# Kernel optimization log

Measured on AMD Instinct MI355X. Metric: run time of the kernel, lower is better.

The kernel has to match this reference:

```python
import jax, jax.numpy as jnp
import numpy as np

N = 100000      # nodes
E = 300000      # edges
D_IN = 32       # input feature dim
D_MEM = 256     # memory dim
D_HID = 256     # hidden dim
D_TIME = 32     # time encoding dim
HEADS = 4
C = D_HID // 4  # per-head channels (GATConv out_channels)
D_OUT = 2


def gru_cell(x, h, wih, whh, bih, bhh):
    # torch.nn.GRUCell semantics, gate order (r, z, n)
    gi = x @ wih.T + bih
    gh = h @ whh.T + bhh
    ir, iz, inn = jnp.split(gi, 3, axis=-1)
    hr, hz, hn = jnp.split(gh, 3, axis=-1)
    r = jax.nn.sigmoid(ir + hr)
    z = jax.nn.sigmoid(iz + hz)
    n = jnp.tanh(inn + r * hn)
    return (1.0 - z) * n + z * h


def gat_layer(h, src, dst, W, a_src, a_dst, bias):
    # PyG GATConv(concat=True), default add_self_loops=True, negative_slope=0.2
    n = h.shape[0]
    xh = (h @ W.T).reshape(n, HEADS, C)              # [N,H,C]
    al_s = (xh * a_src).sum(-1)                      # [N,H]
    al_d = (xh * a_dst).sum(-1)                      # [N,H]
    loop = jnp.arange(n, dtype=src.dtype)
    s = jnp.concatenate([src, loop])
    d = jnp.concatenate([dst, loop])
    e = jax.nn.leaky_relu(al_s[s] + al_d[d], 0.2)    # [E+N,H]
    emax = jax.ops.segment_max(e, d, num_segments=n)
    ee = jnp.exp(e - emax[d])
    denom = jax.ops.segment_sum(ee, d, num_segments=n)
    alpha = ee / denom[d]                            # softmax over incoming edges
    out = jax.ops.segment_sum(alpha[:, :, None] * xh[s], d, num_segments=n)
    return out.reshape(n, HEADS * C) + bias


def setup_inputs() -> dict:
    key = jax.random.key(0)
    ks = jax.random.split(key, 32)
    w = lambda k, sh: jax.random.normal(k, sh, jnp.float32) * 0.05
    d_msg_in = 2 * D_MEM + D_IN + D_TIME  # 576
    return {
        "x": jax.random.normal(ks[0], (N, D_IN), jnp.float32),
        "timestamps": jax.random.uniform(ks[1], (E,), jnp.float32),
        "node_memory": jnp.zeros((N, D_MEM), jnp.float32),
        "last_update_time": jnp.zeros((N,), jnp.float32),
        "msg_w1": w(ks[2], (D_HID, d_msg_in)), "msg_b1": w(ks[3], (D_HID,)),
        "msg_w2": w(ks[4], (D_MEM, D_HID)), "msg_b2": w(ks[5], (D_MEM,)),
        "time_w1": w(ks[6], (D_TIME, 1)), "time_b1": w(ks[7], (D_TIME,)),
        "time_w2": w(ks[8], (D_TIME, D_TIME)), "time_b2": w(ks[9], (D_TIME,)),
        "gru_wih": w(ks[10], (3 * D_MEM, D_MEM)), "gru_whh": w(ks[11], (3 * D_MEM, D_MEM)),
        "gru_bih": w(ks[12], (3 * D_MEM,)), "gru_bhh": w(ks[13], (3 * D_MEM,)),
        "gat1_w": w(ks[14], (HEADS * C, D_MEM)), "gat1_asrc": w(ks[15], (HEADS, C)),
        "gat1_adst": w(ks[16], (HEADS, C)), "gat1_b": w(ks[17], (HEADS * C,)),
        "gat2_w": w(ks[18], (HEADS * C, D_HID)), "gat2_asrc": w(ks[19], (HEADS, C)),
        "gat2_adst": w(ks[20], (HEADS, C)), "gat2_b": w(ks[21], (HEADS * C,)),
        "cls_w1": w(ks[22], (D_HID // 2, D_HID)), "cls_b1": w(ks[23], (D_HID // 2,)),
        "cls_w2": w(ks[24], (D_OUT, D_HID // 2)), "cls_b2": w(ks[25], (D_OUT,)),
        "edge_index": jax.random.randint(ks[26], (2, E), 0, N, jnp.int32),
        "batch": jnp.zeros((N,), jnp.int32),
    }


def reference(x, timestamps, node_memory, last_update_time,
              msg_w1, msg_b1, msg_w2, msg_b2,
              time_w1, time_b1, time_w2, time_b2,
              gru_wih, gru_whh, gru_bih, gru_bhh,
              gat1_w, gat1_asrc, gat1_adst, gat1_b,
              gat2_w, gat2_asrc, gat2_adst, gat2_b,
              cls_w1, cls_b1, cls_w2, cls_b2,
              edge_index, batch):
    src, dst = edge_index[0], edge_index[1]
    edge_attr = x[src]                               # torch path: edge_attr=None -> x[edge_index[0]]
    current_time = timestamps.max()
    # --- compute_messages ---
    dt = (current_time - jnp.maximum(last_update_time[src], last_update_time[dst]))[:, None]
    te = jax.nn.relu(dt @ time_w1.T + time_b1) @ time_w2.T + time_b2
    mi = jnp.concatenate([node_memory[src], node_memory[dst], edge_attr, te], axis=-1)  # [E,576]
    msgs = jax.nn.relu(mi @ msg_w1.T + msg_b1) @ msg_w2.T + msg_b2                      # [E,256]
    # --- update_memory: fused segment-mean + batched GRU ---
    counts = jax.ops.segment_sum(jnp.ones((E,), msgs.dtype), dst, num_segments=N)
    agg = jax.ops.segment_sum(msgs, dst, num_segments=N) / jnp.maximum(counts, 1.0)[:, None]
    mem_new = gru_cell(agg, node_memory, gru_wih, gru_whh, gru_bih, gru_bhh)
    mem = jnp.where((counts > 0)[:, None], mem_new, node_memory)
    # --- GAT embedding layers (dropout inactive in eval) ---
    h = jax.nn.elu(gat_layer(mem, src, dst, gat1_w, gat1_asrc, gat1_adst, gat1_b))
    h = jax.nn.elu(gat_layer(h, src, dst, gat2_w, gat2_asrc, gat2_adst, gat2_b))
    # --- global mean pool (single graph, batch==0) + classifier ---
    gsum = jax.ops.segment_sum(h, batch, num_segments=1)
    gcnt = jax.ops.segment_sum(jnp.ones((N,), h.dtype), batch, num_segments=1)
    g = gsum / gcnt[:, None]
    logits = jax.nn.relu(g @ cls_w1.T + cls_b1) @ cls_w2.T + cls_b2
    return logits
```

## Files before the change

### kernel.cpp

```cpp
#include <hip/hip_runtime.h>

#define NN 100000
#define NE 300000
#define GPLANE 528

typedef float f32x4 __attribute__((ext_vector_type(4)));
typedef __bf16 bf16x8 __attribute__((ext_vector_type(8)));
typedef unsigned short ushort8v __attribute__((ext_vector_type(8)));

__device__ __forceinline__ int enc_f(float f) {
    int i = __float_as_int(f);
    return i >= 0 ? i : (i ^ 0x7fffffff);
}
__device__ __forceinline__ float dec_f(int i) {
    return __int_as_float(i >= 0 ? i : (i ^ 0x7fffffff));
}
__device__ __forceinline__ unsigned short f2bf(float f) {
    unsigned u = __float_as_uint(f);
    u += 0x7fffu + ((u >> 16) & 1u);
    return (unsigned short)(u >> 16);
}
__device__ __forceinline__ float bf2f(unsigned short u) {
    return __uint_as_float((unsigned)u << 16);
}

__global__ void k_dbg(float* out, float v) { out[0] = v; out[1] = v; }

__global__ void k_fill_i32(int* p, int v, int n) {
    int i = blockIdx.x * 256 + threadIdx.x;
    if (i < n) p[i] = v;
}

__global__ void k_pack_w_sub(const float* __restrict__ src, unsigned short* __restrict__ dst,
                             int OUT, int K, int stride, int off) {
    int i = blockIdx.x * 256 + threadIdx.x;
    if (i >= OUT * K) return;
    int o = i / K, k = i % K;
    int ob = o >> 6, n = (o >> 4) & 3, fr = o & 15;
    int step = k >> 5, kq = (k >> 3) & 3, j = k & 7;
    size_t dsti = ((((size_t)step * (OUT >> 6) + ob) * 4 + n) * 64 + (kq * 16 + fr)) * 8 + j;
    dst[dsti] = f2bf(src[(size_t)o * stride + off + k]);
}

__global__ void k_fold_te(const float* __restrict__ msg_w1, const float* __restrict__ tw2,
                          const float* __restrict__ tb2, const float* __restrict__ b1,
                          float* __restrict__ Mtd, float* __restrict__ b1eff) {
    int i = blockIdx.x * 256 + threadIdx.x;
    if (i < 256 * 32) {
        int o = i >> 5, col = i & 31;
        float s = 0.f;
        const float* w1d = msg_w1 + (size_t)o * 576 + 544;
#pragma unroll
        for (int c = 0; c < 32; ++c) s += w1d[c] * tw2[c * 32 + col];
        Mtd[i] = s;
        if (col == 0) {
            float sb = b1[o];
#pragma unroll
            for (int c = 0; c < 32; ++c) sb += w1d[c] * tb2[c];
            b1eff[o] = sb;
        }
    }
}

__global__ void k_timemax(const float* __restrict__ ts, int n, int* out) {
    float m = -INFINITY;
    int stride = gridDim.x * blockDim.x;
    for (int i = blockIdx.x * blockDim.x + threadIdx.x; i < n; i += stride)
        m = fmaxf(m, ts[i]);
    atomicMax(out, enc_f(m));
}

__global__ void k_counts(const int* __restrict__ ei, float* __restrict__ counts) {
    int stride = gridDim.x * blockDim.x;
    for (int i = blockIdx.x * blockDim.x + threadIdx.x; i < NE; i += stride)
        atomicAdd(&counts[ei[NE + i]], 1.f);
}

__global__ void k_scan1(const float* __restrict__ counts, int* __restrict__ rowptr,
                        int* __restrict__ bsum) {
    __shared__ int sh[256];
    int t = threadIdx.x;
    int i = blockIdx.x * 256 + t;
    int v = (i < NN) ? ((int)counts[i] + 1) : 0;
    sh[t] = v;
    __syncthreads();
    for (int off = 1; off < 256; off <<= 1) {
        int x = (t >= off) ? sh[t - off] : 0;
        __syncthreads();
        sh[t] += x;
        __syncthreads();
    }
    if (i < NN) rowptr[i + 1] = sh[t];
    if (t == 255) bsum[blockIdx.x] = sh[255];
}

__global__ void k_scan2(int* __restrict__ bsum, int nb) {
    __shared__ int sh[512];
    int t = threadIdx.x;
    sh[t] = (t < nb) ? bsum[t] : 0;
    __syncthreads();
    for (int off = 1; off < 512; off <<= 1) {
        int x = (t >= off) ? sh[t - off] : 0;
        __syncthreads();
        sh[t] += x;
        __syncthreads();
    }
    if (t < nb) bsum[t] = sh[t];
}

__global__ void k_scan3(int* __restrict__ rowptr, const int* __restrict__ bsum,
                        int* __restrict__ fillp, int* __restrict__ fillE) {
    int i = blockIdx.x * 256 + threadIdx.x;
    if (i == 0) {
        rowptr[0] = 0;
        fillp[0] = 0;
        fillE[0] = 0;
    }
    if (i < NN) {
        int b = i >> 8;
        int off = b > 0 ? bsum[b - 1] : 0;
        int v = rowptr[i + 1] + off;
        rowptr[i + 1] = v;
        if (i + 1 < NN) {
            fillp[i + 1] = v;
            fillE[i + 1] = v - (i + 1);
        }
    }
}

__global__ void k_csr_fill(const int* __restrict__ ei, int* __restrict__ fill,
                           int* __restrict__ colidx) {
    int i = blockIdx.x * 256 + threadIdx.x;
    if (i < NE) {
        int d = ei[NE + i];
        int pos = atomicAdd(&fill[d], 1);
        colidx[pos] = ei[i];
    } else if (i < NE + NN) {
        int n = i - NE;
        int pos = atomicAdd(&fill[n], 1);
        colidx[pos] = n;
    }
}

__global__ void k_ecsr_fill(const int* __restrict__ ei, int* __restrict__ fillE,
                            int* __restrict__ esrc, int* __restrict__ edst) {
    int i = blockIdx.x * 256 + threadIdx.x;
    if (i < NE) {
        int d = ei[NE + i];
        int pos = atomicAdd(&fillE[d], 1);
        esrc[pos] = ei[i];
        edst[pos] = d;
    }
}

__global__ __launch_bounds__(512, 4) void k_pre1(
    const float* __restrict__ mem, const float* __restrict__ x,
    const unsigned short* __restrict__ w1ap, const unsigned short* __restrict__ w1bp,
    const unsigned short* __restrict__ w1cp,
    unsigned short* __restrict__ P13, unsigned short* __restrict__ P2,
    unsigned short* __restrict__ membf) {
    __shared__ unsigned short Af[2 * 8 * GPLANE];
    __shared__ unsigned short Axf[2 * 512];
    const int t = threadIdx.x;
    const int lane = t & 63, w = t >> 6;
    const int row0 = blockIdx.x * 32;
    const int frow = lane & 15, hi = lane >> 4;
    const int half = w >> 2, cq = w & 3;

    {
        int sr = t >> 4, sq = t & 15;
        int row = row0 + sr;
        const float* pm = mem + (size_t)row * 256 + sq * 16;
        int smq = sr >> 4, sfr = sr & 15;
#pragma unroll
        for (int j2 = 0; j2 < 2; ++j2) {
            int k8 = sq * 16 + j2 * 8;
            int st = k8 >> 5, kq = (k8 >> 3) & 3;
            float4 m0 = *(const float4*)(pm + j2 * 8);
            float4 m1 = *(const float4*)(pm + j2 * 8 + 4);
            ushort8v um;
            um[0] = f2bf(m0.x); um[1] = f2bf(m0.y); um[2] = f2bf(m0.z); um[3] = f2bf(m0.w);
            um[4] = f2bf(m1.x); um[5] = f2bf(m1.y); um[6] = f2bf(m1.z); um[7] = f2bf(m1.w);
            *(ushort8v*)&Af[((smq * 8) + st) * GPLANE + (kq * 16 + sfr) * 8] = um;
            *(ushort8v*)(membf + (size_t)row * 256 + k8) = um;
        }
    }
    if (t < 128) {
        int sr = t >> 2, sq = t & 3;
        int row = row0 + sr;
        const float* px = x + (size_t)row * 32 + sq * 8;
        float4 v0 = *(const float4*)px, v1 = *(const float4*)(px + 4);
        ushort8v u;
        u[0] = f2bf(v0.x); u[1] = f2bf(v0.y); u[2] = f2bf(v0.z); u[3] = f2bf(v0.w);
        u[4] = f2bf(v1.x); u[5] = f2bf(v1.y); u[6] = f2bf(v1.z); u[7] = f2bf(v1.w);
        *(ushort8v*)&Axf[(sr >> 4) * 512 + (sq * 16 + (sr & 15)) * 8] = u;
    }
    __syncthreads();

    f32x4 acc[2][4];
#pragma unroll
    for (int mf = 0; mf < 2; ++mf)
#pragma unroll
        for (int c = 0; c < 4; ++c) acc[mf][c] = (f32x4){0, 0, 0, 0};

    const unsigned short* wp = half ? w1bp : w1ap;
    for (int step = 0; step < 8; ++step) {
        bf16x8 aA[2];
#pragma unroll
        for (int mf = 0; mf < 2; ++mf)
            aA[mf] = *(const bf16x8*)&Af[((mf * 8) + step) * GPLANE + lane * 8];
#pragma unroll
        for (int ctl = 0; ctl < 4; ++ctl) {
            bf16x8 b = *(const bf16x8*)(wp + (((size_t)step * 4 + cq) * 4 + ctl) * 512 + lane * 8);
#pragma unroll
            for (int mf = 0; mf < 2; ++mf)
                acc[mf][ctl] = __builtin_amdgcn_mfma_f32_16x16x32_bf16(aA[mf], b, acc[mf][ctl], 0, 0, 0);
        }
    }
    if (half == 0) {
        bf16x8 aX[2];
#pragma unroll
        for (int mf = 0; mf < 2; ++mf)
            aX[mf] = *(const bf16x8*)&Axf[mf * 512 + lane * 8];
#pragma unroll
        for (int ctl = 0; ctl < 4; ++ctl) {
            bf16x8 b = *(const bf16x8*)(w1cp + (((size_t)0 * 4 + cq) * 4 + ctl) * 512 + lane * 8);
#pragma unroll
            for (int mf = 0; mf < 2; ++mf)
                acc[mf][ctl] = __builtin_amdgcn_mfma_f32_16x16x32_bf16(aX[mf], b, acc[mf][ctl], 0, 0, 0);
        }
    }
    unsigned short* P = half ? P2 : P13;
#pragma unroll
    for (int mf = 0; mf < 2; ++mf)
#pragma unroll
        for (int ctl = 0; ctl < 4; ++ctl) {
            int col = cq * 64 + ctl * 16 + frow;
#pragma unroll
            for (int r = 0; r < 4; ++r) {
                int row = row0 + mf * 16 + hi * 4 + r;
                P[(size_t)row * 256 + col] = f2bf(acc[mf][ctl][r]);
            }
        }
}

__global__ __launch_bounds__(512, 4) void k_msg_mfma(
    const int* __restrict__ ct, const float* __restrict__ lut,
    const int* __restrict__ esrc, const int* __restrict__ edst,
    const unsigned short* __restrict__ P13, const unsigned short* __restrict__ P2,
    const unsigned short* __restrict__ wtdp, const float* __restrict__ b1eff,
    const unsigned short* __restrict__ w2p, const float* __restrict__ b2,
    const float* __restrict__ tw1, const float* __restrict__ tb1,
    float* __restrict__ agg) {
    __shared__ unsigned short As[64][40];
    __shared__ unsigned short Hs[64][264];
    __shared__ int Da[64];

    const int t = threadIdx.x;
    const int lane = t & 63, wave = t >> 6;
    const int row0 = blockIdx.x * 64;
    const int frow = lane & 15;
    const int fk = (lane >> 4) * 8;
    const int hi = lane >> 4;
    const int wb = wave >> 1;
    const int wn = (wave & 1) * 2;

    if (t < 64) {
        int e = row0 + t;
        Da[t] = (e < NE) ? edst[e] : -1;
    }

    const int srow = t >> 3;
    const int sj = t & 7;
    const int eIdx = row0 + srow;
    const bool ev = eIdx < NE;
    const int s_e = ev ? esrc[eIdx] : 0;
    const int d_e = ev ? edst[eIdx] : 0;

    {
        float ctv = dec_f(*ct);
        float dt = ev ? (ctv - fmaxf(lut[s_e], lut[d_e])) : 0.f;
        ushort4 u;
        int c0 = sj * 4;
        u.x = f2bf(fmaxf(dt * tw1[c0 + 0] + tb1[c0 + 0], 0.f));
        u.y = f2bf(fmaxf(dt * tw1[c0 + 1] + tb1[c0 + 1], 0.f));
        u.z = f2bf(fmaxf(dt * tw1[c0 + 2] + tb1[c0 + 2], 0.f));
        u.w = f2bf(fmaxf(dt * tw1[c0 + 3] + tb1[c0 + 3], 0.f));
        *(ushort4*)&As[srow][c0] = u;
    }
#pragma unroll
    for (int q = 0; q < 4; ++q) {
        int c = sj * 8 + q * 64;
        ushort4 a0 = *(const ushort4*)(P13 + (size_t)s_e * 256 + c);
        ushort4 a1 = *(const ushort4*)(P13 + (size_t)s_e * 256 + c + 4);
        ushort4 b0 = *(const ushort4*)(P2 + (size_t)d_e * 256 + c);
        ushort4 b1v = *(const ushort4*)(P2 + (size_t)d_e * 256 + c + 4);
        ushort8v u;
        u[0] = f2bf(bf2f(a0.x) + bf2f(b0.x)); u[1] = f2bf(bf2f(a0.y) + bf2f(b0.y));
        u[2] = f2bf(bf2f(a0.z) + bf2f(b0.z)); u[3] = f2bf(bf2f(a0.w) + bf2f(b0.w));
        u[4] = f2bf(bf2f(a1.x) + bf2f(b1v.x)); u[5] = f2bf(bf2f(a1.y) + bf2f(b1v.y));
        u[6] = f2bf(bf2f(a1.z) + bf2f(b1v.z)); u[7] = f2bf(bf2f(a1.w) + bf2f(b1v.w));
        *(ushort8v*)&Hs[srow][c] = u;
    }
    __syncthreads();

    f32x4 acc[4][2];
#pragma unroll
    for (int m = 0; m < 4; m++)
#pragma unroll
        for (int n = 0; n < 2; n++) acc[m][n] = (f32x4){0.f, 0.f, 0.f, 0.f};

    {
        bf16x8 a[4];
#pragma unroll
        for (int m = 0; m < 4; m++)
            a[m] = *(const bf16x8*)&As[m * 16 + frow][fk];
#pragma unroll
        for (int n = 0; n < 2; n++) {
            bf16x8 b = *(const bf16x8*)(wtdp + (((size_t)0 * 4 + wb) * 4 + (wn + n)) * 512 + lane * 8);
#pragma unroll
            for (int m = 0; m < 4; m++)
                acc[m][n] = __builtin_amdgcn_mfma_f32_16x16x32_bf16(a[m], b, acc[m][n], 0, 0, 0);
        }
    }
#pragma unroll
    for (int n = 0; n < 2; n++) {
        int c = wave * 32 + n * 16 + frow;
        float bb = b1eff[c];
#pragma unroll
        for (int m = 0; m < 4; m++) {
#pragma unroll
            for (int r = 0; r < 4; r++) {
                int rr = m * 16 + hi * 4 + r;
                float v = acc[m][n][r] + bf2f(Hs[rr][c]) + bb;
                Hs[rr][c] = f2bf(fmaxf(v, 0.f));
            }
            acc[m][n] = (f32x4){0.f, 0.f, 0.f, 0.f};
        }
    }
    __syncthreads();

    bf16x8 bnext[2];
#pragma unroll
    for (int n = 0; n < 2; n++)
        bnext[n] = *(const bf16x8*)(w2p + (((size_t)0 * 4 + wb) * 4 + (wn + n)) * 512 + lane * 8);
    for (int step = 0; step < 8; ++step) {
        const int k0 = step * 32;
        bf16x8 bcur[2];
#pragma unroll
        for (int n = 0; n < 2; n++) bcur[n] = bnext[n];
        if (step < 7) {
#pragma unroll
            for (int n = 0; n < 2; n++)
                bnext[n] = *(const bf16x8*)(w2p + (((size_t)(step + 1) * 4 + wb) * 4 + (wn + n)) * 512 + lane * 8);
        }
        bf16x8 a[4];
#pragma unroll
        for (int m = 0; m < 4; m++)
            a[m] = *(const bf16x8*)&Hs[m * 16 + frow][k0 + fk];
#pragma unroll
        for (int m = 0; m < 4; m++)
#pragma unroll
            for (int n = 0; n < 2; n++)
                acc[m][n] = __builtin_amdgcn_mfma_f32_16x16x32_bf16(a[m], bcur[n], acc[m][n], 0, 0, 0);
    }

    __syncthreads();
    {
        float bb2[2];
#pragma unroll
        for (int n = 0; n < 2; n++) bb2[n] = b2[wave * 32 + n * 16 + frow];
#pragma unroll
        for (int m = 0; m < 4; m++) {
            int rbase = m * 16 + hi * 4;
#pragma unroll
            for (int r = 0; r < 4; r++) {
#pragma unroll
                for (int n = 0; n < 2; n++)
                    Hs[rbase + r][wave * 32 + n * 16 + frow] = f2bf(acc[m][n][r] + bb2[n]);
            }
        }
        __syncthreads();

        int nrows = min(64, NE - row0);
        int col = t & 255;
        int rs = (t >> 8) * 32;
        int re = min(nrows, rs + 32);
        if (rs < re) {
            float run = 0.f;
            int cur = Da[rs];
            for (int i = rs; i < re; ++i) {
                int d = Da[i];
                if (d != cur) {
                    atomicAdd(agg + (size_t)cur * 256 + col, run);
                    run = 0.f;
                    cur = d;
                }
                run += bf2f(Hs[i][col]);
            }
            atomicAdd(agg + (size_t)cur * 256 + col, run);
        }
    }
}

__global__ __launch_bounds__(512, 4) void k_gru_mfma(
    const float* __restrict__ agg, const unsigned short* __restrict__ membf,
    const float* __restrict__ counts,
    const unsigned short* __restrict__ pwih, const unsigned short* __restrict__ pwhh,
    const float* __restrict__ bih, const float* __restrict__ bhh,
    unsigned short* __restrict__ memout) {
    __shared__ unsigned short Af[2 * 2 * 8 * GPLANE];
    const int t = threadIdx.x;
    const int lane = t & 63, w = t >> 6;
    const int row0 = blockIdx.x * 32;
    const int frow = lane & 15, hi = lane >> 4;
    const int cqp = blockIdx.y * 2 + (w >> 2);
    const int ctl = w & 3;

    {
        int sr = t >> 4, sq = t & 15;
        int row = row0 + sr;
        float inv = 1.f / fmaxf(counts[row], 1.f);
        const float* pa = agg + (size_t)row * 256 + sq * 16;
        const unsigned short* pm = membf + (size_t)row * 256 + sq * 16;
        int smq = sr >> 4, sfr = sr & 15;
#pragma unroll
        for (int j2 = 0; j2 < 2; ++j2) {
            int k8 = sq * 16 + j2 * 8;
            int st = k8 >> 5, kq = (k8 >> 3) & 3;
            float4 a0 = *(const float4*)(pa + j2 * 8);
            float4 a1 = *(const float4*)(pa + j2 * 8 + 4);
            ushort8v um = *(const ushort8v*)(pm + j2 * 8);
            ushort8v ua;
            ua[0] = f2bf(a0.x * inv); ua[1] = f2bf(a0.y * inv); ua[2] = f2bf(a0.z * inv); ua[3] = f2bf(a0.w * inv);
            ua[4] = f2bf(a1.x * inv); ua[5] = f2bf(a1.y * inv); ua[6] = f2bf(a1.z * inv); ua[7] = f2bf(a1.w * inv);
            int pos = kq * 16 + sfr;
            *(ushort8v*)&Af[(((0 * 2 + smq) * 8) + st) * GPLANE + pos * 8] = ua;
            *(ushort8v*)&Af[(((1 * 2 + smq) * 8) + st) * GPLANE + pos * 8] = um;
        }
    }
    __syncthreads();

    f32x4 rpre[2], zpre[2], inn[2], hn[2];
#pragma unroll
    for (int mf = 0; mf < 2; ++mf) {
        rpre[mf] = (f32x4){0, 0, 0, 0};
        zpre[mf] = (f32x4){0, 0, 0, 0};
        inn[mf]  = (f32x4){0, 0, 0, 0};
        hn[mf]   = (f32x4){0, 0, 0, 0};
    }

    for (int step = 0; step < 8; ++step) {
        bf16x8 aA[2], aM[2];
#pragma unroll
        for (int mf = 0; mf < 2; ++mf) {
            aA[mf] = *(const bf16x8*)&Af[(((0 * 2 + mf) * 8) + step) * GPLANE + lane * 8];
            aM[mf] = *(const bf16x8*)&Af[(((1 * 2 + mf) * 8) + step) * GPLANE + lane * 8];
        }
        size_t o_r = (((size_t)step * 12 + 0 * 4 + cqp) * 4 + ctl) * 512 + lane * 8;
        size_t o_z = (((size_t)step * 12 + 1 * 4 + cqp) * 4 + ctl) * 512 + lane * 8;
        size_t o_n = (((size_t)step * 12 + 2 * 4 + cqp) * 4 + ctl) * 512 + lane * 8;
        bf16x8 bIr = *(const bf16x8*)(pwih + o_r);
        bf16x8 bHr = *(const bf16x8*)(pwhh + o_r);
        bf16x8 bIz = *(const bf16x8*)(pwih + o_z);
        bf16x8 bHz = *(const bf16x8*)(pwhh + o_z);
        bf16x8 bIn = *(const bf16x8*)(pwih + o_n);
        bf16x8 bHn = *(const bf16x8*)(pwhh + o_n);
#pragma unroll
        for (int mf = 0; mf < 2; ++mf) {
            rpre[mf] = __builtin_amdgcn_mfma_f32_16x16x32_bf16(aA[mf], bIr, rpre[mf], 0, 0, 0);
            rpre[mf] = __builtin_amdgcn_mfma_f32_16x16x32_bf16(aM[mf], bHr, rpre[mf], 0, 0, 0);
            zpre[mf] = __builtin_amdgcn_mfma_f32_16x16x32_bf16(aA[mf], bIz, zpre[mf], 0, 0, 0);
            zpre[mf] = __builtin_amdgcn_mfma_f32_16x16x32_bf16(aM[mf], bHz, zpre[mf], 0, 0, 0);
            inn[mf]  = __builtin_amdgcn_mfma_f32_16x16x32_bf16(aA[mf], bIn, inn[mf], 0, 0, 0);
            hn[mf]   = __builtin_amdgcn_mfma_f32_16x16x32_bf16(aM[mf], bHn, hn[mf], 0, 0, 0);
        }
    }

    const int col = cqp * 64 + ctl * 16 + frow;
    const float br = bih[col] + bhh[col];
    const float bz = bih[256 + col] + bhh[256 + col];
    const float bin = bih[512 + col];
    const float bhn = bhh[512 + col];
#pragma unroll
    for (int mf = 0; mf < 2; ++mf)
#pragma unroll
        for (int r = 0; r < 4; ++r) {
            int row = row0 + mf * 16 + hi * 4 + r;
            float cnt = counts[row];
            float rg = 1.f / (1.f + expf(-(rpre[mf][r] + br)));
            float zg = 1.f / (1.f + expf(-(zpre[mf][r] + bz)));
            float ng = tanhf(inn[mf][r] + bin + rg * (hn[mf][r] + bhn));
            int pos = ((col >> 3) & 3) * 16 + (hi * 4 + r);
            float hp = bf2f(Af[(((1 * 2 + mf) * 8) + (col >> 5)) * GPLANE + pos * 8 + (col & 7)]);
            memout[(size_t)row * 256 + col] = f2bf((cnt > 0.f) ? ((1.f - zg) * ng + zg * hp) : hp);
        }
}

__global__ __launch_bounds__(256, 4) void k_xh_mfma(
    const unsigned short* __restrict__ A, const unsigned short* __restrict__ wp,
    const float* __restrict__ asrc, const float* __restrict__ adst,
    unsigned short* __restrict__ xh, float* __restrict__ als, float* __restrict__ ald) {
    const int t = threadIdx.x;
    const int lane = t & 63, w = t >> 6;
    const int row0 = blockIdx.x * 64;
    const int frow = lane & 15, fk = (lane >> 4) * 8, hi = lane >> 4;

    f32x4 acc[4][4];
#pragma unroll
    for (int m = 0; m < 4; m++)
#pragma unroll
        for (int c = 0; c < 4; c++) acc[m][c] = (f32x4){0, 0, 0, 0};

    for (int step = 0; step < 8; ++step) {
        const int k0 = step * 32;
        bf16x8 a[4];
#pragma unroll
        for (int m = 0; m < 4; ++m) {
            int row = min(row0 + m * 16 + frow, NN - 1);
            a[m] = *(const bf16x8*)(A + (size_t)row * 256 + k0 + fk);
        }
#pragma unroll
        for (int ctl = 0; ctl < 4; ++ctl) {
            bf16x8 b = *(const bf16x8*)(wp + (((size_t)step * 4 + w) * 4 + ctl) * 512 + lane * 8);
#pragma unroll
            for (int m = 0; m < 4; ++m)
                acc[m][ctl] = __builtin_amdgcn_mfma_f32_16x16x32_bf16(a[m], b, acc[m][ctl], 0, 0, 0);
        }
    }

    float asv[4], adv[4];
#pragma unroll
    for (int ctl = 0; ctl < 4; ++ctl) {
        asv[ctl] = asrc[w * 64 + ctl * 16 + frow];
        adv[ctl] = adst[w * 64 + ctl * 16 + frow];
    }
#pragma unroll
    for (int m = 0; m < 4; ++m) {
        float ps[4] = {0, 0, 0, 0}, pd[4] = {0, 0, 0, 0};
#pragma unroll
        for (int ctl = 0; ctl < 4; ++ctl) {
            int col = w * 64 + ctl * 16 + frow;
#pragma unroll
            for (int r = 0; r < 4; ++r) {
                float v = acc[m][ctl][r];
                ps[r] += v * asv[ctl];
                pd[r] += v * adv[ctl];
                int row = row0 + m * 16 + hi * 4 + r;
                if (row < NN) xh[(size_t)row * 256 + col] = f2bf(v);
            }
        }
#pragma unroll
        for (int off = 1; off < 16; off <<= 1) {
#pragma unroll
            for (int r = 0; r < 4; ++r) {
                ps[r] += __shfl_xor(ps[r], off, 64);
                pd[r] += __shfl_xor(pd[r], off, 64);
            }
        }
        if (frow == 0) {
#pragma unroll
            for (int r = 0; r < 4; ++r) {
                int row = row0 + m * 16 + hi * 4 + r;
                if (row < NN) { als[row * 4 + w] = ps[r]; ald[row * 4 + w] = pd[r]; }
            }
        }
    }
}

__global__ __launch_bounds__(256) void k_gat_csr(
    const int* __restrict__ rowptr, const int* __restrict__ colidx,
    const float* __restrict__ als, const float* __restrict__ ald,
    const unsigned short* __restrict__ xh, const float* __restrict__ bias,
    unsigned short* __restrict__ outb) {
    int d = blockIdx.x * 4 + (threadIdx.x >> 6);
    if (d >= NN) return;
    int lane = threadIdx.x & 63;
    int h = lane >> 4;
    int beg = rowptr[d], end = rowptr[d + 1];
    float aldv = ald[d * 4 + h];

    float m = -INFINITY;
    for (int p = beg; p < end; ++p) {
        int s = colidx[p];
        float e = als[s * 4 + h] + aldv;
        e = e > 0.f ? e : 0.2f * e;
        m = fmaxf(m, e);
    }
    float den = 0.f;
    float a0 = 0.f, a1 = 0.f, a2 = 0.f, a3 = 0.f;
    for (int p = beg; p < end; ++p) {
        int s = colidx[p];
        float e = als[s * 4 + h] + aldv;
        e = e > 0.f ? e : 0.2f * e;
        float pw = expf(e - m);
        den += pw;
        ushort4 uv = *(const ushort4*)(xh + (size_t)s * 256 + lane * 4);
        a0 += pw * bf2f(uv.x);
        a1 += pw * bf2f(uv.y);
        a2 += pw * bf2f(uv.z);
        a3 += pw * bf2f(uv.w);
    }
    float inv = 1.f / den;
    int c = lane * 4;
    float4 bv = *(const float4*)(bias + c);
    float ox = a0 * inv + bv.x; ox = ox > 0.f ? ox : expm1f(ox);
    float oy = a1 * inv + bv.y; oy = oy > 0.f ? oy : expm1f(oy);
    float oz = a2 * inv + bv.z; oz = oz > 0.f ? oz : expm1f(oz);
    float ow = a3 * inv + bv.w; ow = ow > 0.f ? ow : expm1f(ow);
    ushort4 o;
    o.x = f2bf(ox); o.y = f2bf(oy); o.z = f2bf(oz); o.w = f2bf(ow);
    *(ushort4*)(outb + (size_t)d * 256 + c) = o;
}

__global__ __launch_bounds__(256) void k_pool(const unsigned short* __restrict__ h,
                                              const int* __restrict__ batch, float* __restrict__ gsum) {
    int t = threadIdx.x;
    const int per = (NN + gridDim.x - 1) / gridDim.x;
    int n0 = blockIdx.x * per, n1 = min(NN, n0 + per);
    float s = 0.f, cnt = 0.f;
    for (int n = n0; n < n1; n++) {
        if (batch[n] == 0) {
            s += bf2f(h[(size_t)n * 256 + t]);
            cnt += 1.f;
        }
    }
    atomicAdd(&gsum[t], s);
    if (t == 0) atomicAdd(&gsum[256], cnt);
}

__global__ void k_cls(const float* __restrict__ gsum, const float* __restrict__ w1,
                      const float* __restrict__ b1, const float* __restrict__ w2,
                      const float* __restrict__ b2, float* __restrict__ out) {
    __shared__ float g[256];
    __shared__ float hid[128];
    int t = threadIdx.x;
    float gc = gsum[256];
    g[t] = gsum[t] / gc;
    __syncthreads();
    if (t < 128) {
        float s = b1[t];
        for (int k = 0; k < 256; k++) s += g[k] * w1[t * 256 + k];
        hid[t] = fmaxf(s, 0.f);
    }
    __syncthreads();
    if (t < 2) {
        float s = b2[t];
        for (int k = 0; k < 128; k++) s += hid[k] * w2[t * 128 + k];
        out[t] = s;
    }
}

extern "C" void kernel_launch(void* const* d_in, const int* in_sizes, int n_in,
                              void* d_out, int out_size, void* d_ws, size_t ws_size,
                              hipStream_t stream) {
    const float* xv      = (const float*)d_in[0];
    const float* tsv     = (const float*)d_in[1];
    const float* nodemem = (const float*)d_in[2];
    const float* lut     = (const float*)d_in[3];
    const float* msg_w1  = (const float*)d_in[4];
    const float* msg_b1  = (const float*)d_in[5];
    const float* msg_w2  = (const float*)d_in[6];
    const float* msg_b2  = (const float*)d_in[7];
    const float* time_w1 = (const float*)d_in[8];
    const float* time_b1 = (const float*)d_in[9];
    const float* time_w2 = (const float*)d_in[10];
    const float* time_b2 = (const float*)d_in[11];
    const float* gru_wih = (const float*)d_in[12];
    const float* gru_whh = (const float*)d_in[13];
    const float* gru_bih = (const float*)d_in[14];
    const float* gru_bhh = (const float*)d_in[15];
    const float* gat1_w    = (const float*)d_in[16];
    const float* gat1_asrc = (const float*)d_in[17];
    const float* gat1_adst = (const float*)d_in[18];
    const float* gat1_b    = (const float*)d_in[19];
    const float* gat2_w    = (const float*)d_in[20];
    const float* gat2_asrc = (const float*)d_in[21];
    const float* gat2_adst = (const float*)d_in[22];
    const float* gat2_b    = (const float*)d_in[23];
    const float* cls_w1 = (const float*)d_in[24];
    const float* cls_b1 = (const float*)d_in[25];
    const float* cls_w2 = (const float*)d_in[26];
    const float* cls_b2 = (const float*)d_in[27];
    const int* ei    = (const int*)d_in[28];
    const int* batch = (const int*)d_in[29];
    float* out = (float*)d_out;

    char* wsb = (char*)d_ws;
    size_t off = 0;
    auto carve = [&](size_t bytes) {
        char* p = wsb + off;
        off += (bytes + 255) & ~(size_t)255;
        return p;
    };
    int*   curtime = (int*)carve(4);
    unsigned short* w1ap = (unsigned short*)carve((size_t)256 * 256 * 2);
    unsigned short* w1bp = (unsigned short*)carve((size_t)256 * 256 * 2);
    unsigned short* w1cp = (unsigned short*)carve((size_t)256 * 32 * 2);
    unsigned short* wtdp = (unsigned short*)carve((size_t)256 * 32 * 2);
    unsigned short* w2p  = (unsigned short*)carve((size_t)256 * 256 * 2);
    unsigned short* wihp = (unsigned short*)carve((size_t)768 * 256 * 2);
    unsigned short* whhp = (unsigned short*)carve((size_t)768 * 256 * 2);
    unsigned short* g1p  = (unsigned short*)carve((size_t)256 * 256 * 2);
    unsigned short* g2p  = (unsigned short*)carve((size_t)256 * 256 * 2);
    float* Mtd   = (float*)carve((size_t)256 * 32 * 4);
    float* b1eff = (float*)carve(256 * 4);
    unsigned short* P13  = (unsigned short*)carve((size_t)NN * 256 * 2);
    unsigned short* P2   = (unsigned short*)carve((size_t)NN * 256 * 2);
    unsigned short* membf = (unsigned short*)carve((size_t)NN * 256 * 2);
    float* als    = (float*)carve((size_t)NN * 4 * 4);
    float* ald    = (float*)carve((size_t)NN * 4 * 4);
    float* counts = (float*)carve((size_t)NN * 4);
    float* gsum   = (float*)carve(257 * 4);
    int*   rowptr = (int*)carve((size_t)(NN + 1) * 4);
    int*   colidx = (int*)carve((size_t)(NE + NN) * 4);
    int*   fillp  = (int*)carve((size_t)NN * 4);
    int*   bsum   = (int*)carve(512 * 4);
    int*   esrc   = (int*)carve((size_t)NE * 4);
    int*   edst   = (int*)carve((size_t)NE * 4);
    int*   fillE  = (int*)carve((size_t)NN * 4);
    float* R1     = (float*)carve((size_t)NN * 256 * 4);
    float* R2     = (float*)carve((size_t)NN * 256 * 4);

    if (ws_size < off) {
        k_dbg<<<1, 1, 0, stream>>>(out, (float)(ws_size >> 20));
        return;
    }

    float* agg   = R1;
    unsigned short* memo  = (unsigned short*)R2;
    unsigned short* xh1   = (unsigned short*)R1;
    unsigned short* xh2   = (unsigned short*)R1;
    unsigned short* outb1 = (unsigned short*)R2;
    unsigned short* outb2 = (unsigned short*)R2;

    hipMemsetAsync(agg, 0, (size_t)NN * 256 * 4, stream);
    hipMemsetAsync(counts, 0, (size_t)NN * 4, stream);
    hipMemsetAsync(gsum, 0, 257 * 4, stream);
    k_fill_i32<<<1, 256, 0, stream>>>(curtime, (int)0x80000000, 1);

    k_fold_te<<<32, 256, 0, stream>>>(msg_w1, time_w2, time_b2, msg_b1, Mtd, b1eff);
    k_pack_w_sub<<<256, 256, 0, stream>>>(msg_w1, w1ap, 256, 256, 576, 0);
    k_pack_w_sub<<<256, 256, 0, stream>>>(msg_w1, w1bp, 256, 256, 576, 256);
    k_pack_w_sub<<<32, 256, 0, stream>>>(msg_w1, w1cp, 256, 32, 576, 512);
    k_pack_w_sub<<<32, 256, 0, stream>>>(Mtd, wtdp, 256, 32, 32, 0);
    k_pack_w_sub<<<256, 256, 0, stream>>>(msg_w2, w2p, 256, 256, 256, 0);
    k_pack_w_sub<<<768, 256, 0, stream>>>(gru_wih, wihp, 768, 256, 256, 0);
    k_pack_w_sub<<<768, 256, 0, stream>>>(gru_whh, whhp, 768, 256, 256, 0);
    k_pack_w_sub<<<256, 256, 0, stream>>>(gat1_w, g1p, 256, 256, 256, 0);
    k_pack_w_sub<<<256, 256, 0, stream>>>(gat2_w, g2p, 256, 256, 256, 0);

    k_counts<<<1024, 256, 0, stream>>>(ei, counts);
    k_scan1<<<391, 256, 0, stream>>>(counts, rowptr, bsum);
    k_scan2<<<1, 512, 0, stream>>>(bsum, 391);
    k_scan3<<<391, 256, 0, stream>>>(rowptr, bsum, fillp, fillE);
    k_csr_fill<<<1563, 256, 0, stream>>>(ei, fillp, colidx);
    k_ecsr_fill<<<1172, 256, 0, stream>>>(ei, fillE, esrc, edst);

    k_timemax<<<512, 256, 0, stream>>>(tsv, NE, curtime);
    k_pre1<<<3125, 512, 0, stream>>>(nodemem, xv, w1ap, w1bp, w1cp, P13, P2, membf);
    k_msg_mfma<<<4688, 512, 0, stream>>>(curtime, lut, esrc, edst, P13, P2,
                                         wtdp, b1eff, w2p, msg_b2,
                                         time_w1, time_b1, agg);
    k_gru_mfma<<<dim3(3125, 2), 512, 0, stream>>>(agg, membf, counts, wihp, whhp,
                                                  gru_bih, gru_bhh, memo);

    k_xh_mfma<<<1563, 256, 0, stream>>>(memo, g1p, gat1_asrc, gat1_adst, xh1, als, ald);
    k_gat_csr<<<25000, 256, 0, stream>>>(rowptr, colidx, als, ald, xh1, gat1_b, outb1);

    k_xh_mfma<<<1563, 256, 0, stream>>>(outb1, g2p, gat2_asrc, gat2_adst, xh2, als, ald);
    k_gat_csr<<<25000, 256, 0, stream>>>(rowptr, colidx, als, ald, xh2, gat2_b, outb2);

    k_pool<<<2048, 256, 0, stream>>>(outb2, batch, gsum);
    k_cls<<<1, 256, 0, stream>>>(gsum, cls_w1, cls_b1, cls_w2, cls_b2, out);
}
```

Baseline: 810.2 us.

## Cover all GRU output columns per block instead of splitting across grid y

The GRU kernel previously ran a 2-wide grid in y, with each block handling half of the 256 output columns. That meant every 32-row tile's agg and memory inputs were loaded and staged into shared memory twice. Now each wave computes two column fragments, so a single block covers all columns and the A staging and bf16 conversion happen once per row tile. The trade-off is doubled accumulator registers per thread (32 f32x4 vectors) under launch_bounds(512,4), which risks spills or lower occupancy.

```diff
diff --git a/kernel.cpp b/kernel.cpp
--- a/kernel.cpp
+++ b/kernel.cpp
@@ -414,8 +414,6 @@
     const int lane = t & 63, w = t >> 6;
     const int row0 = blockIdx.x * 32;
     const int frow = lane & 15, hi = lane >> 4;
-    const int cqp = blockIdx.y * 2 + (w >> 2);
-    const int ctl = w & 3;
 
     {
         int sr = t >> 4, sq = t & 15;
@@ -441,14 +439,16 @@
     }
     __syncthreads();
 
-    f32x4 rpre[2], zpre[2], inn[2], hn[2];
-#pragma unroll
-    for (int mf = 0; mf < 2; ++mf) {
-        rpre[mf] = (f32x4){0, 0, 0, 0};
-        zpre[mf] = (f32x4){0, 0, 0, 0};
-        inn[mf]  = (f32x4){0, 0, 0, 0};
-        hn[mf]   = (f32x4){0, 0, 0, 0};
-    }
+    f32x4 rpre[2][2], zpre[2][2], inn[2][2], hn[2][2];
+#pragma unroll
+    for (int n = 0; n < 2; ++n)
+#pragma unroll
+        for (int mf = 0; mf < 2; ++mf) {
+            rpre[n][mf] = (f32x4){0, 0, 0, 0};
+            zpre[n][mf] = (f32x4){0, 0, 0, 0};
+            inn[n][mf]  = (f32x4){0, 0, 0, 0};
+            hn[n][mf]   = (f32x4){0, 0, 0, 0};
+        }
 
     for (int step = 0; step < 8; ++step) {
         bf16x8 aA[2], aM[2];
@@ -457,44 +457,54 @@
             aA[mf] = *(const bf16x8*)&Af[(((0 * 2 + mf) * 8) + step) * GPLANE + lane * 8];
             aM[mf] = *(const bf16x8*)&Af[(((1 * 2 + mf) * 8) + step) * GPLANE + lane * 8];
         }
-        size_t o_r = (((size_t)step * 12 + 0 * 4 + cqp) * 4 + ctl) * 512 + lane * 8;
-        size_t o_z = (((size_t)step * 12 + 1 * 4 + cqp) * 4 + ctl) * 512 + lane * 8;
-        size_t o_n = (((size_t)step * 12 + 2 * 4 + cqp) * 4 + ctl) * 512 + lane * 8;
-        bf16x8 bIr = *(const bf16x8*)(pwih + o_r);
-        bf16x8 bHr = *(const bf16x8*)(pwhh + o_r);
-        bf16x8 bIz = *(const bf16x8*)(pwih + o_z);
-        bf16x8 bHz = *(const bf16x8*)(pwhh + o_z);
-        bf16x8 bIn = *(const bf16x8*)(pwih + o_n);
-        bf16x8 bHn = *(const bf16x8*)(pwhh + o_n);
-#pragma unroll
-        for (int mf = 0; mf < 2; ++mf) {
-            rpre[mf] = __builtin_amdgcn_mfma_f32_16x16x32_bf16(aA[mf], bIr, rpre[mf], 0, 0, 0);
-            rpre[mf] = __builtin_amdgcn_mfma_f32_16x16x32_bf16(aM[mf], bHr, rpre[mf], 0, 0, 0);
-            zpre[mf] = __builtin_amdgcn_mfma_f32_16x16x32_bf16(aA[mf], bIz, zpre[mf], 0, 0, 0);
-            zpre[mf] = __builtin_amdgcn_mfma_f32_16x16x32_bf16(aM[mf], bHz, zpre[mf], 0, 0, 0);
-            inn[mf]  = __builtin_amdgcn_mfma_f32_16x16x32_bf16(aA[mf], bIn, inn[mf], 0, 0, 0);
-            hn[mf]   = __builtin_amdgcn_mfma_f32_16x16x32_bf16(aM[mf], bHn, hn[mf], 0, 0, 0);
-        }
-    }
-
-    const int col = cqp * 64 + ctl * 16 + frow;
-    const float br = bih[col] + bhh[col];
-    const float bz = bih[256 + col] + bhh[256 + col];
-    const float bin = bih[512 + col];
-    const float bhn = bhh[512 + col];
-#pragma unroll
-    for (int mf = 0; mf < 2; ++mf)
-#pragma unroll
-        for (int r = 0; r < 4; ++r) {
-            int row = row0 + mf * 16 + hi * 4 + r;
-            float cnt = counts[row];
-            float rg = 1.f / (1.f + expf(-(rpre[mf][r] + br)));
-            float zg = 1.f / (1.f + expf(-(zpre[mf][r] + bz)));
-            float ng = tanhf(inn[mf][r] + bin + rg * (hn[mf][r] + bhn));
-            int pos = ((col >> 3) & 3) * 16 + (hi * 4 + r);
-            float hp = bf2f(Af[(((1 * 2 + mf) * 8) + (col >> 5)) * GPLANE + pos * 8 + (col & 7)]);
-            memout[(size_t)row * 256 + col] = f2bf((cnt > 0.f) ? ((1.f - zg) * ng + zg * hp) : hp);
-        }
+#pragma unroll
+        for (int n = 0; n < 2; ++n) {
+            int fi = w * 2 + n;
+            int cqp = fi >> 2, ctl = fi & 3;
+            size_t o_r = (((size_t)step * 12 + 0 * 4 + cqp) * 4 + ctl) * 512 + lane * 8;
+            size_t o_z = (((size_t)step * 12 + 1 * 4 + cqp) * 4 + ctl) * 512 + lane * 8;
+            size_t o_n = (((size_t)step * 12 + 2 * 4 + cqp) * 4 + ctl) * 512 + lane * 8;
+            bf16x8 bIr = *(const bf16x8*)(pwih + o_r);
+            bf16x8 bHr = *(const bf16x8*)(pwhh + o_r);
+            bf16x8 bIz = *(const bf16x8*)(pwih + o_z);
+            bf16x8 bHz = *(const bf16x8*)(pwhh + o_z);
+            bf16x8 bIn = *(const bf16x8*)(pwih + o_n);
+            bf16x8 bHn = *(const bf16x8*)(pwhh + o_n);
+#pragma unroll
+            for (int mf = 0; mf < 2; ++mf) {
+                rpre[n][mf] = __builtin_amdgcn_mfma_f32_16x16x32_bf16(aA[mf], bIr, rpre[n][mf], 0, 0, 0);
+                rpre[n][mf] = __builtin_amdgcn_mfma_f32_16x16x32_bf16(aM[mf], bHr, rpre[n][mf], 0, 0, 0);
+                zpre[n][mf] = __builtin_amdgcn_mfma_f32_16x16x32_bf16(aA[mf], bIz, zpre[n][mf], 0, 0, 0);
+                zpre[n][mf] = __builtin_amdgcn_mfma_f32_16x16x32_bf16(aM[mf], bHz, zpre[n][mf], 0, 0, 0);
+                inn[n][mf]  = __builtin_amdgcn_mfma_f32_16x16x32_bf16(aA[mf], bIn, inn[n][mf], 0, 0, 0);
+                hn[n][mf]   = __builtin_amdgcn_mfma_f32_16x16x32_bf16(aM[mf], bHn, hn[n][mf], 0, 0, 0);
+            }
+        }
+    }
+
+#pragma unroll
+    for (int n = 0; n < 2; ++n) {
+        int fi = w * 2 + n;
+        int cqp = fi >> 2, ctl = fi & 3;
+        const int col = cqp * 64 + ctl * 16 + frow;
+        const float br = bih[col] + bhh[col];
+        const float bz = bih[256 + col] + bhh[256 + col];
+        const float bin = bih[512 + col];
+        const float bhn = bhh[512 + col];
+#pragma unroll
+        for (int mf = 0; mf < 2; ++mf)
+#pragma unroll
+            for (int r = 0; r < 4; ++r) {
+                int row = row0 + mf * 16 + hi * 4 + r;
+                float cnt = counts[row];
+                float rg = 1.f / (1.f + expf(-(rpre[n][mf][r] + br)));
+                float zg = 1.f / (1.f + expf(-(zpre[n][mf][r] + bz)));
+                float ng = tanhf(inn[n][mf][r] + bin + rg * (hn[n][mf][r] + bhn));
+                int pos = ((col >> 3) & 3) * 16 + (hi * 4 + r);
+                float hp = bf2f(Af[(((1 * 2 + mf) * 8) + (col >> 5)) * GPLANE + pos * 8 + (col & 7)]);
+                memout[(size_t)row * 256 + col] = f2bf((cnt > 0.f) ? ((1.f - zg) * ng + zg * hp) : hp);
+            }
+    }
 }
 
 __global__ __launch_bounds__(256, 4) void k_xh_mfma(
@@ -762,8 +772,8 @@
     k_msg_mfma<<<4688, 512, 0, stream>>>(curtime, lut, esrc, edst, P13, P2,
                                          wtdp, b1eff, w2p, msg_b2,
                                          time_w1, time_b1, agg);
-    k_gru_mfma<<<dim3(3125, 2), 512, 0, stream>>>(agg, membf, counts, wihp, whhp,
-                                                  gru_bih, gru_bhh, memo);
+    k_gru_mfma<<<3125, 512, 0, stream>>>(agg, membf, counts, wihp, whhp,
+                                         gru_bih, gru_bhh, memo);
 
     k_xh_mfma<<<1563, 256, 0, stream>>>(memo, g1p, gat1_asrc, gat1_adst, xh1, als, ald);
     k_gat_csr<<<25000, 256, 0, stream>>>(rowptr, colidx, als, ald, xh1, gat1_b, outb1);
```

After: 822.0 us. No clear change (+1.5%).
